# Kernel tuning notes

Measured on AMD Instinct MI355X. Metric: run time of the kernel, lower is better.

## Reference

```python
import jax, jax.numpy as jnp
import numpy as np

N_VERTS = 100000
N_EDGES = 50000
NNZ = 1600000
C_IN = 128
C_OUT = 128


def setup_inputs() -> dict:
    key = jax.random.key(0)
    k = jax.random.split(key, 7)
    X = jax.random.normal(k[0], (N_VERTS, C_IN), dtype=jnp.float32)
    v_ids = jax.random.randint(k[1], (NNZ,), 0, N_VERTS)
    e_ids = jax.random.randint(k[2], (NNZ,), 0, N_EDGES)
    s1 = 1.0 / np.sqrt(C_IN)
    s2 = 1.0 / np.sqrt(C_OUT)
    W_v2e = jax.random.uniform(k[3], (C_IN, C_OUT), jnp.float32, -s1, s1)
    b_v2e = jax.random.uniform(k[4], (C_OUT,), jnp.float32, -s1, s1)
    W_e2v = jax.random.uniform(k[5], (C_OUT, C_OUT), jnp.float32, -s2, s2)
    b_e2v = jax.random.uniform(k[6], (C_OUT,), jnp.float32, -s2, s2)
    return {"X": X, "W_v2e": W_v2e, "b_v2e": b_v2e, "W_e2v": W_e2v,
            "b_e2v": b_e2v, "v_ids": v_ids, "e_ids": e_ids}


def _mean_agg(feats_src, src_ids, dst_ids, num_dst):
    # gather source features along incidence list, segment-mean into destination
    gathered = feats_src[src_ids]                                   # [nnz, C]
    ssum = jax.ops.segment_sum(gathered, dst_ids, num_segments=num_dst)
    cnt = jax.ops.segment_sum(jnp.ones((src_ids.shape[0],), feats_src.dtype),
                              dst_ids, num_segments=num_dst)
    return ssum / jnp.maximum(cnt, 1.0)[:, None]


def reference(X, W_v2e, b_v2e, W_e2v, b_e2v, v_ids, e_ids):
    # theta_v2e
    Xp = X @ W_v2e + b_v2e                                          # [V, C_out]
    # v2e mean aggregation + ReLU
    Y = jax.nn.relu(_mean_agg(Xp, v_ids, e_ids, N_EDGES))           # [E, C_out]
    # theta_e2v
    Yp = Y @ W_e2v + b_e2v                                          # [E, C_out]
    # e2v mean aggregation
    Xo = _mean_agg(Yp, e_ids, v_ids, N_VERTS)                       # [V, C_out]
    # not is_last: final ReLU (bn disabled, dropout in eval mode = identity)
    return jax.nn.relu(Xo)
```

## Files before the change

kernel.cpp:

```cpp
#include <hip/hip_runtime.h>
#include <stdint.h>

#define V_N 100000
#define E_N 50000
#define C_N 128

#define NB_E 196
#define NB_V 391
#define NBINS (NB_E + NB_V)
#define CHUNK 8192
#define CAP_B 10240

typedef unsigned short u16;
typedef unsigned int u32;

__device__ __forceinline__ u16 f2bf(float f) {
    union { float f; u32 i; } c; c.f = f;
    u32 i = c.i;
    i += 0x7fffu + ((i >> 16) & 1u);
    return (u16)(i >> 16);
}
__device__ __forceinline__ void unpack2(u32 u, float& lo, float& hi) {
    union { u32 i; float f; } a, b;
    a.i = u << 16; b.i = u & 0xffff0000u;
    lo = a.f; hi = b.f;
}

__global__ __launch_bounds__(64) void flagf_k(float* out, float v) {
    if (threadIdx.x == 0 && blockIdx.x == 0) out[0] = v;
}

__global__ __launch_bounds__(256) void zero_i4(int4* __restrict__ p, int n) {
    int i = blockIdx.x * 256 + threadIdx.x;
    if (i < n) { int4 z = {0, 0, 0, 0}; p[i] = z; }
}

__global__ __launch_bounds__(256) void histA_k(const int* __restrict__ v_ids,
                                               const int* __restrict__ e_ids,
                                               int* __restrict__ gbin, int nnz) {
    __shared__ int hb[NBINS];
    for (int i = threadIdx.x; i < NBINS; i += 256) hb[i] = 0;
    __syncthreads();
    const int nnz4 = nnz >> 2;
    const int b4 = blockIdx.x * (CHUNK >> 2);
    #pragma unroll
    for (int u = 0; u < 8; ++u) {
        int i4 = b4 + u * 256 + threadIdx.x;
        if (i4 < nnz4) {
            int4 e = ((const int4*)e_ids)[i4];
            int4 v = ((const int4*)v_ids)[i4];
            #define HA(ee, vv) \
                if ((unsigned)ee < (unsigned)E_N && (unsigned)vv < (unsigned)V_N) { \
                    atomicAdd(&hb[ee >> 8], 1); atomicAdd(&hb[NB_E + (vv >> 8)], 1); }
            HA(e.x, v.x); HA(e.y, v.y); HA(e.z, v.z); HA(e.w, v.w);
            #undef HA
        }
    }
    __syncthreads();
    for (int i = threadIdx.x; i < NBINS; i += 256)
        if (hb[i]) atomicAdd(&gbin[i], hb[i]);
}

__global__ __launch_bounds__(1024) void scanB_k(const int* __restrict__ gbin,
                                                int* __restrict__ base_e, int* __restrict__ base_v,
                                                int* __restrict__ curb_e, int* __restrict__ curb_v,
                                                int* __restrict__ off_e, int* __restrict__ off_v) {
    __shared__ int wtot[16];
    const int t = threadIdx.x, lane = t & 63, wid = t >> 6;
    {
        int x = (t < NB_E) ? gbin[t] : 0;
        int incl = x;
        for (int d = 1; d < 64; d <<= 1) { int u = __shfl_up(incl, d); if (lane >= d) incl += u; }
        if (lane == 63) wtot[wid] = incl;
        __syncthreads();
        int carry = 0;
        for (int w = 0; w < wid; ++w) carry += wtot[w];
        int excl = carry + incl - x;
        if (t < NB_E) { base_e[t] = excl; curb_e[t] = excl; }
        if (t == 0) {
            int tot = 0;
            for (int w = 0; w < 16; ++w) tot += wtot[w];
            base_e[NB_E] = tot; off_e[E_N] = tot;
        }
        __syncthreads();
    }
    {
        int x = (t < NB_V) ? gbin[NB_E + t] : 0;
        int incl = x;
        for (int d = 1; d < 64; d <<= 1) { int u = __shfl_up(incl, d); if (lane >= d) incl += u; }
        if (lane == 63) wtot[wid] = incl;
        __syncthreads();
        int carry = 0;
        for (int w = 0; w < wid; ++w) carry += wtot[w];
        int excl = carry + incl - x;
        if (t < NB_V) { base_v[t] = excl; curb_v[t] = excl; }
        if (t == 0) {
            int tot = 0;
            for (int w = 0; w < 16; ++w) tot += wtot[w];
            base_v[NB_V] = tot; off_v[V_N] = tot;
        }
    }
}

__global__ __launch_bounds__(512) void passA_k(const int* __restrict__ v_ids,
                                               const int* __restrict__ e_ids,
                                               int* __restrict__ curb_e, int* __restrict__ curb_v,
                                               u32* __restrict__ pairs_e, u32* __restrict__ pairs_v,
                                               int nnz) {
    __shared__ u32 stage[CHUNK];
    __shared__ int cnt[512], runoff[513], delta[512], cnt2[512];
    __shared__ int wtot[8];
    const int t = threadIdx.x, lane = t & 63, wid = t >> 6;
    const int nnz4 = nnz >> 2;
    const int b4 = blockIdx.x * (CHUNK >> 2);

    for (int dir = 0; dir < 2; ++dir) {
        const int nb = dir ? NB_V : NB_E;
        for (int i = t; i < nb; i += 512) { cnt[i] = 0; cnt2[i] = 0; }
        __syncthreads();
        #pragma unroll
        for (int u = 0; u < 4; ++u) {
            int i4 = b4 + u * 512 + t;
            if (i4 < nnz4) {
                int4 e = ((const int4*)e_ids)[i4];
                int4 v = ((const int4*)v_ids)[i4];
                #define PC(ee, vv) \
                    if ((unsigned)ee < (unsigned)E_N && (unsigned)vv < (unsigned)V_N) { \
                        int k_ = dir ? vv : ee; atomicAdd(&cnt[k_ >> 8], 1); }
                PC(e.x, v.x); PC(e.y, v.y); PC(e.z, v.z); PC(e.w, v.w);
                #undef PC
            }
        }
        __syncthreads();
        int x = (t < nb) ? cnt[t] : 0;
        int incl = x;
        for (int d = 1; d < 64; d <<= 1) { int u = __shfl_up(incl, d); if (lane >= d) incl += u; }
        if (lane == 63) wtot[wid] = incl;
        __syncthreads();
        int carry = 0;
        for (int w = 0; w < wid; ++w) carry += wtot[w];
        int excl = carry + incl - x;
        if (t < nb) runoff[t] = excl;
        if (t == 0) {
            int tot = 0;
            for (int w = 0; w < 8; ++w) tot += wtot[w];
            runoff[nb] = tot;
        }
        __syncthreads();
        const int total = runoff[nb];
        if (t < nb && cnt[t] > 0) {
            int r = atomicAdd((dir ? curb_v : curb_e) + t, cnt[t]);
            delta[t] = r - runoff[t];
        }
        __syncthreads();
        #pragma unroll
        for (int u = 0; u < 4; ++u) {
            int i4 = b4 + u * 512 + t;
            if (i4 < nnz4) {
                int4 e = ((const int4*)e_ids)[i4];
                int4 v = ((const int4*)v_ids)[i4];
                #define PS(ee, vv) \
                    if ((unsigned)ee < (unsigned)E_N && (unsigned)vv < (unsigned)V_N) { \
                        int k_ = dir ? vv : ee; int b_ = k_ >> 8; \
                        u32 pk_ = dir ? (((u32)(k_ & 255) << 16) | (u32)ee) \
                                      : (((u32)(k_ & 255) << 17) | (u32)vv); \
                        int idx_ = runoff[b_] + atomicAdd(&cnt2[b_], 1); \
                        stage[idx_] = pk_; }
                PS(e.x, v.x); PS(e.y, v.y); PS(e.z, v.z); PS(e.w, v.w);
                #undef PS
            }
        }
        __syncthreads();
        u32* pairs = dir ? pairs_v : pairs_e;
        for (int i = t; i < total; i += 512) {
            int lo = 0, hi = nb;
            while (hi - lo > 1) { int mid = (lo + hi) >> 1; if (runoff[mid] <= i) lo = mid; else hi = mid; }
            pairs[i + delta[lo]] = stage[i];
        }
        __syncthreads();
    }
}

__global__ __launch_bounds__(256) void passB_k(const u32* __restrict__ pairs_e,
                                               const u32* __restrict__ pairs_v,
                                               const int* __restrict__ base_e,
                                               const int* __restrict__ base_v,
                                               int* __restrict__ off_e, int* __restrict__ off_v,
                                               int* __restrict__ se_src, int* __restrict__ sv_src) {
    __shared__ int cntk[256], curk[256];
    __shared__ u32 buf[CAP_B];
    __shared__ int wtot[4];
    int b = blockIdx.x;
    const u32* pairs; const int* base; int* off; int* outv; int keyN, shift; u32 mask;
    if (b < NB_E) { pairs = pairs_e; base = base_e; off = off_e; outv = se_src; keyN = E_N; shift = 17; mask = 0x1FFFFu; }
    else { b -= NB_E; pairs = pairs_v; base = base_v; off = off_v; outv = sv_src; keyN = V_N; shift = 16; mask = 0xFFFFu; }
    const int lo = base[b], hi = base[b + 1], cnt = hi - lo, k0 = b << 8;
    const int t = threadIdx.x, lane = t & 63, wid = t >> 6;
    cntk[t] = 0;
    __syncthreads();
    for (int i = t; i < cnt; i += 256) { u32 p = pairs[lo + i]; atomicAdd(&cntk[p >> shift], 1); }
    __syncthreads();
    int x = cntk[t];
    int incl = x;
    for (int d = 1; d < 64; d <<= 1) { int u = __shfl_up(incl, d); if (lane >= d) incl += u; }
    if (lane == 63) wtot[wid] = incl;
    __syncthreads();
    int carry = 0;
    for (int w = 0; w < wid; ++w) carry += wtot[w];
    int excl = carry + incl - x;
    if (k0 + t < keyN) off[k0 + t] = lo + excl;
    curk[t] = excl;
    __syncthreads();
    if (cnt <= CAP_B) {
        for (int i = t; i < cnt; i += 256) {
            u32 p = pairs[lo + i];
            int pos = atomicAdd(&curk[p >> shift], 1);
            buf[pos] = p & mask;
        }
        __syncthreads();
        for (int i = t; i < cnt; i += 256) outv[lo + i] = (int)buf[i];
    } else {
        for (int i = t; i < cnt; i += 256) {
            u32 p = pairs[lo + i];
            int pos = atomicAdd(&curk[p >> shift], 1);
            outv[lo + pos] = (int)(p & mask);
        }
    }
}

template<int MODE>
__global__ __launch_bounds__(256) void gemm_tiled_k(const float* __restrict__ A,
                                                    const float* __restrict__ W,
                                                    const float* __restrict__ bias,
                                                    const int* __restrict__ off,
                                                    u16* __restrict__ Cout, int M) {
    __shared__ float As[128 * 32];
    __shared__ float Wsh[32 * 128];
    const int tid = threadIdx.x;
    const int tx = tid & 15;
    const int ty = tid >> 4;
    const int m0 = blockIdx.x * 128;

    float acc[8][8];
    #pragma unroll
    for (int i = 0; i < 8; ++i)
        #pragma unroll
        for (int j = 0; j < 8; ++j) acc[i][j] = 0.f;

    for (int kk = 0; kk < 128; kk += 32) {
        __syncthreads();
        #pragma unroll
        for (int u = 0; u < 4; ++u) {
            int f = tid + u * 256;
            int r = f >> 3, c4 = f & 7;
            float4 val = { 0.f, 0.f, 0.f, 0.f };
            if (m0 + r < M) {
                val = *(const float4*)(A + (size_t)(m0 + r) * C_N + kk + c4 * 4);
                if (MODE) {
                    val.x = fmaxf(val.x, 0.f); val.y = fmaxf(val.y, 0.f);
                    val.z = fmaxf(val.z, 0.f); val.w = fmaxf(val.w, 0.f);
                }
            }
            int sc4 = c4 ^ ((r >> 3) & 7);
            *(float4*)(As + r * 32 + sc4 * 4) = val;
        }
        #pragma unroll
        for (int u = 0; u < 4; ++u) {
            int f = tid + u * 256;
            int r = f >> 5, c4 = f & 31;
            *(float4*)(Wsh + r * 128 + c4 * 4) = *(const float4*)(W + (size_t)(kk + r) * C_N + c4 * 4);
        }
        __syncthreads();
        #pragma unroll
        for (int k4 = 0; k4 < 32; k4 += 4) {
            float4 a[8];
            #pragma unroll
            for (int i = 0; i < 8; ++i) {
                int row = ty * 8 + i;
                int sc4 = (k4 >> 2) ^ (ty & 7);
                a[i] = *(const float4*)(As + row * 32 + sc4 * 4);
            }
            #pragma unroll
            for (int dk = 0; dk < 4; ++dk) {
                float4 w0 = *(const float4*)(Wsh + (k4 + dk) * 128 + tx * 4);
                float4 w1 = *(const float4*)(Wsh + (k4 + dk) * 128 + 64 + tx * 4);
                #pragma unroll
                for (int i = 0; i < 8; ++i) {
                    float av = (dk == 0) ? a[i].x : (dk == 1) ? a[i].y : (dk == 2) ? a[i].z : a[i].w;
                    acc[i][0] = fmaf(av, w0.x, acc[i][0]);
                    acc[i][1] = fmaf(av, w0.y, acc[i][1]);
                    acc[i][2] = fmaf(av, w0.z, acc[i][2]);
                    acc[i][3] = fmaf(av, w0.w, acc[i][3]);
                    acc[i][4] = fmaf(av, w1.x, acc[i][4]);
                    acc[i][5] = fmaf(av, w1.y, acc[i][5]);
                    acc[i][6] = fmaf(av, w1.z, acc[i][6]);
                    acc[i][7] = fmaf(av, w1.w, acc[i][7]);
                }
            }
        }
    }

    float4 bb0 = *(const float4*)(bias + tx * 4);
    float4 bb1 = *(const float4*)(bias + 64 + tx * 4);
    #pragma unroll
    for (int i = 0; i < 8; ++i) {
        int m = m0 + ty * 8 + i;
        if (m >= M) break;
        float inv = 1.f;
        if (MODE) { int len = off[m + 1] - off[m]; inv = 1.f / (float)max(len, 1); }
        float v0, v1, v2, v3, v4, v5, v6, v7;
        if (MODE) {
            v0 = acc[i][0] * inv + bb0.x; v1 = acc[i][1] * inv + bb0.y;
            v2 = acc[i][2] * inv + bb0.z; v3 = acc[i][3] * inv + bb0.w;
            v4 = acc[i][4] * inv + bb1.x; v5 = acc[i][5] * inv + bb1.y;
            v6 = acc[i][6] * inv + bb1.z; v7 = acc[i][7] * inv + bb1.w;
        } else {
            v0 = acc[i][0] + bb0.x; v1 = acc[i][1] + bb0.y;
            v2 = acc[i][2] + bb0.z; v3 = acc[i][3] + bb0.w;
            v4 = acc[i][4] + bb1.x; v5 = acc[i][5] + bb1.y;
            v6 = acc[i][6] + bb1.z; v7 = acc[i][7] + bb1.w;
        }
        u32 p0 = (u32)f2bf(v0) | ((u32)f2bf(v1) << 16);
        u32 p1 = (u32)f2bf(v2) | ((u32)f2bf(v3) << 16);
        u32 p2 = (u32)f2bf(v4) | ((u32)f2bf(v5) << 16);
        u32 p3 = (u32)f2bf(v6) | ((u32)f2bf(v7) << 16);
        u32* dst = (u32*)(Cout + (size_t)m * C_N);
        uint2 q0 = { p0, p1 }, q1 = { p2, p3 };
        *(uint2*)(dst + tx * 2) = q0;
        *(uint2*)(dst + 32 + tx * 2) = q1;
    }
}

__global__ __launch_bounds__(256) void seg_e_k(const u16* __restrict__ Xp,
                                               const int* __restrict__ off,
                                               const int* __restrict__ srcs,
                                               float* __restrict__ Ysum, int E) {
    int e = blockIdx.x * 4 + (threadIdx.x >> 6);
    if (e >= E) return;
    int lane = threadIdx.x & 63;
    int j0 = off[e], j1 = off[e + 1];
    float a0 = 0.f, a1 = 0.f;
    int j = j0;
    for (; j + 1 < j1; j += 2) {
        int s0 = srcs[j], s1 = srcs[j + 1];
        u32 q0 = ((const u32*)(Xp + (size_t)s0 * C_N))[lane];
        u32 q1 = ((const u32*)(Xp + (size_t)s1 * C_N))[lane];
        float l0, h0, l1, h1;
        unpack2(q0, l0, h0); unpack2(q1, l1, h1);
        a0 += l0 + l1; a1 += h0 + h1;
    }
    if (j < j1) {
        int s0 = srcs[j];
        u32 q0 = ((const u32*)(Xp + (size_t)s0 * C_N))[lane];
        float l0, h0; unpack2(q0, l0, h0);
        a0 += l0; a1 += h0;
    }
    float2 w; w.x = a0; w.y = a1;
    ((float2*)Ysum)[(size_t)e * 64 + lane] = w;
}

__global__ __launch_bounds__(256) void seg_v_k(const u16* __restrict__ Yp,
                                               const int* __restrict__ off,
                                               const int* __restrict__ srcs,
                                               float* __restrict__ out, int V) {
    int v = blockIdx.x * 4 + (threadIdx.x >> 6);
    if (v >= V) return;
    int lane = threadIdx.x & 63;
    int j0 = off[v], j1 = off[v + 1];
    float a0 = 0.f, a1 = 0.f;
    int j = j0;
    for (; j + 1 < j1; j += 2) {
        int s0 = srcs[j], s1 = srcs[j + 1];
        u32 q0 = ((const u32*)(Yp + (size_t)s0 * C_N))[lane];
        u32 q1 = ((const u32*)(Yp + (size_t)s1 * C_N))[lane];
        float l0, h0, l1, h1;
        unpack2(q0, l0, h0); unpack2(q1, l1, h1);
        a0 += l0 + l1; a1 += h0 + h1;
    }
    if (j < j1) {
        int s0 = srcs[j];
        u32 q0 = ((const u32*)(Yp + (size_t)s0 * C_N))[lane];
        float l0, h0; unpack2(q0, l0, h0);
        a0 += l0; a1 += h0;
    }
    float inv = 1.0f / (float)max(j1 - j0, 1);
    float2 w;
    w.x = fmaxf(a0 * inv, 0.f);
    w.y = fmaxf(a1 * inv, 0.f);
    ((float2*)out)[(size_t)v * 64 + lane] = w;
}

extern "C" void kernel_launch(void* const* d_in, const int* in_sizes, int n_in,
                              void* d_out, int out_size, void* d_ws, size_t ws_size,
                              hipStream_t stream) {
    const float* X     = (const float*)d_in[0];
    const float* W_v2e = (const float*)d_in[1];
    const float* b_v2e = (const float*)d_in[2];
    const float* W_e2v = (const float*)d_in[3];
    const float* b_e2v = (const float*)d_in[4];
    const int*   v_ids = (const int*)d_in[5];
    const int*   e_ids = (const int*)d_in[6];
    float* out = (float*)d_out;

    bool sizesOK = (n_in == 7) && (out_size == 12800000)
        && in_sizes[0] == 12800000 && in_sizes[1] == 16384 && in_sizes[2] == 128
        && in_sizes[3] == 16384 && in_sizes[4] == 128
        && in_sizes[5] == 1600000 && in_sizes[6] == 1600000;
    if (!sizesOK) { flagf_k<<<1, 64, 0, stream>>>(out, 1.0e6f); return; }
    if (ws_size < 28000000) { flagf_k<<<1, 64, 0, stream>>>(out, 2.0e6f); return; }
    const int nnz = in_sizes[5];

    u32*   pairs_e = (u32*)d_out;
    u32*   pairs_v = pairs_e + nnz;
    u16*   Xp   = (u16*)d_out;
    float* Ysum = (float*)((char*)d_out + 25600000);

    char* ws = (char*)d_ws;
    u16* Yp     = (u16*)(ws + 0);
    int* se_src = (int*)(ws + 12800000);
    int* sv_src = (int*)(ws + 19200000);
    int* gbin   = (int*)(ws + 25600000);
    int* base_e = (int*)(ws + 25602560);
    int* base_v = (int*)(ws + 25603584);
    int* curb_e = (int*)(ws + 25605632);
    int* curb_v = (int*)(ws + 25606656);
    int* off_e  = (int*)(ws + 25608704);
    int* off_v  = (int*)(ws + 25808768);

    const int NCH = (nnz + CHUNK - 1) / CHUNK;

    zero_i4<<<1, 256, 0, stream>>>((int4*)gbin, 152);
    histA_k<<<NCH, 256, 0, stream>>>(v_ids, e_ids, gbin, nnz);
    scanB_k<<<1, 1024, 0, stream>>>(gbin, base_e, base_v, curb_e, curb_v, off_e, off_v);
    passA_k<<<NCH, 512, 0, stream>>>(v_ids, e_ids, curb_e, curb_v, pairs_e, pairs_v, nnz);
    passB_k<<<NBINS, 256, 0, stream>>>(pairs_e, pairs_v, base_e, base_v, off_e, off_v, se_src, sv_src);

    gemm_tiled_k<0><<<(V_N + 127) / 128, 256, 0, stream>>>(X, W_v2e, b_v2e, nullptr, Xp, V_N);
    seg_e_k<<<(E_N + 3) / 4, 256, 0, stream>>>(Xp, off_e, se_src, Ysum, E_N);
    gemm_tiled_k<1><<<(E_N + 127) / 128, 256, 0, stream>>>(Ysum, W_e2v, b_e2v, off_e, Yp, E_N);
    seg_v_k<<<(V_N + 3) / 4, 256, 0, stream>>>(Yp, off_v, sv_src, out, V_N);

    (void)ws_size;
}
```

Measured before the change: 444.5 us.

## Fuse first GEMM with histogram, stage ids in LDS, widen segment gathers

Merges the first projection GEMM and the incidence histogram into one launch, with block ranges split between the two roles, so the GEMM runs concurrently with the sort preprocessing. To allow this, the pair buffers move to the second half of the output buffer so they no longer overlap Xp. passA now loads the id chunk into shared memory once instead of reading it from global four times, at the cost of much more LDS per block and lower occupancy. The segment-mean kernels are unified, and each half-wave now gathers 8-byte rows so four neighbours are in flight per iteration, with a cross-half shuffle reduction at the end.

```diff
diff --git a/kernel.cpp b/kernel.cpp
--- a/kernel.cpp
+++ b/kernel.cpp
@@ -10,6 +10,7 @@
 #define NBINS (NB_E + NB_V)
 #define CHUNK 8192
 #define CAP_B 10240
+#define G1B 782
 
 typedef unsigned short u16;
 typedef unsigned int u32;
@@ -35,30 +36,154 @@
     if (i < n) { int4 z = {0, 0, 0, 0}; p[i] = z; }
 }
 
-__global__ __launch_bounds__(256) void histA_k(const int* __restrict__ v_ids,
-                                               const int* __restrict__ e_ids,
-                                               int* __restrict__ gbin, int nnz) {
-    __shared__ int hb[NBINS];
-    for (int i = threadIdx.x; i < NBINS; i += 256) hb[i] = 0;
-    __syncthreads();
-    const int nnz4 = nnz >> 2;
-    const int b4 = blockIdx.x * (CHUNK >> 2);
+template<int MODE>
+__device__ __forceinline__ void gemm_body(float* As, float* Wsh, int bid,
+                                          const float* __restrict__ A,
+                                          const float* __restrict__ W,
+                                          const float* __restrict__ bias,
+                                          const int* __restrict__ off,
+                                          u16* __restrict__ Cout, int M) {
+    const int tid = threadIdx.x;
+    const int tx = tid & 15;
+    const int ty = tid >> 4;
+    const int m0 = bid * 128;
+
+    float acc[8][8];
     #pragma unroll
-    for (int u = 0; u < 8; ++u) {
-        int i4 = b4 + u * 256 + threadIdx.x;
-        if (i4 < nnz4) {
-            int4 e = ((const int4*)e_ids)[i4];
-            int4 v = ((const int4*)v_ids)[i4];
-            #define HA(ee, vv) \
-                if ((unsigned)ee < (unsigned)E_N && (unsigned)vv < (unsigned)V_N) { \
-                    atomicAdd(&hb[ee >> 8], 1); atomicAdd(&hb[NB_E + (vv >> 8)], 1); }
-            HA(e.x, v.x); HA(e.y, v.y); HA(e.z, v.z); HA(e.w, v.w);
-            #undef HA
-        }
-    }
-    __syncthreads();
-    for (int i = threadIdx.x; i < NBINS; i += 256)
-        if (hb[i]) atomicAdd(&gbin[i], hb[i]);
+    for (int i = 0; i < 8; ++i)
+        #pragma unroll
+        for (int j = 0; j < 8; ++j) acc[i][j] = 0.f;
+
+    for (int kk = 0; kk < 128; kk += 32) {
+        __syncthreads();
+        #pragma unroll
+        for (int u = 0; u < 4; ++u) {
+            int f = tid + u * 256;
+            int r = f >> 3, c4 = f & 7;
+            float4 val = { 0.f, 0.f, 0.f, 0.f };
+            if (m0 + r < M) {
+                val = *(const float4*)(A + (size_t)(m0 + r) * C_N + kk + c4 * 4);
+                if (MODE) {
+                    val.x = fmaxf(val.x, 0.f); val.y = fmaxf(val.y, 0.f);
+                    val.z = fmaxf(val.z, 0.f); val.w = fmaxf(val.w, 0.f);
+                }
+            }
+            int sc4 = c4 ^ ((r >> 3) & 7);
+            *(float4*)(As + r * 32 + sc4 * 4) = val;
+        }
+        #pragma unroll
+        for (int u = 0; u < 4; ++u) {
+            int f = tid + u * 256;
+            int r = f >> 5, c4 = f & 31;
+            *(float4*)(Wsh + r * 128 + c4 * 4) = *(const float4*)(W + (size_t)(kk + r) * C_N + c4 * 4);
+        }
+        __syncthreads();
+        #pragma unroll
+        for (int k4 = 0; k4 < 32; k4 += 4) {
+            float4 a[8];
+            #pragma unroll
+            for (int i = 0; i < 8; ++i) {
+                int row = ty * 8 + i;
+                int sc4 = (k4 >> 2) ^ (ty & 7);
+                a[i] = *(const float4*)(As + row * 32 + sc4 * 4);
+            }
+            #pragma unroll
+            for (int dk = 0; dk < 4; ++dk) {
+                float4 w0 = *(const float4*)(Wsh + (k4 + dk) * 128 + tx * 4);
+                float4 w1 = *(const float4*)(Wsh + (k4 + dk) * 128 + 64 + tx * 4);
+                #pragma unroll
+                for (int i = 0; i < 8; ++i) {
+                    float av = (dk == 0) ? a[i].x : (dk == 1) ? a[i].y : (dk == 2) ? a[i].z : a[i].w;
+                    acc[i][0] = fmaf(av, w0.x, acc[i][0]);
+                    acc[i][1] = fmaf(av, w0.y, acc[i][1]);
+                    acc[i][2] = fmaf(av, w0.z, acc[i][2]);
+                    acc[i][3] = fmaf(av, w0.w, acc[i][3]);
+                    acc[i][4] = fmaf(av, w1.x, acc[i][4]);
+                    acc[i][5] = fmaf(av, w1.y, acc[i][5]);
+                    acc[i][6] = fmaf(av, w1.z, acc[i][6]);
+                    acc[i][7] = fmaf(av, w1.w, acc[i][7]);
+                }
+            }
+        }
+    }
+
+    float4 bb0 = *(const float4*)(bias + tx * 4);
+    float4 bb1 = *(const float4*)(bias + 64 + tx * 4);
+    #pragma unroll
+    for (int i = 0; i < 8; ++i) {
+        int m = m0 + ty * 8 + i;
+        if (m >= M) break;
+        float inv = 1.f;
+        if (MODE) { int len = off[m + 1] - off[m]; inv = 1.f / (float)max(len, 1); }
+        float v0, v1, v2, v3, v4, v5, v6, v7;
+        if (MODE) {
+            v0 = acc[i][0] * inv + bb0.x; v1 = acc[i][1] * inv + bb0.y;
+            v2 = acc[i][2] * inv + bb0.z; v3 = acc[i][3] * inv + bb0.w;
+            v4 = acc[i][4] * inv + bb1.x; v5 = acc[i][5] * inv + bb1.y;
+            v6 = acc[i][6] * inv + bb1.z; v7 = acc[i][7] * inv + bb1.w;
+        } else {
+            v0 = acc[i][0] + bb0.x; v1 = acc[i][1] + bb0.y;
+            v2 = acc[i][2] + bb0.z; v3 = acc[i][3] + bb0.w;
+            v4 = acc[i][4] + bb1.x; v5 = acc[i][5] + bb1.y;
+            v6 = acc[i][6] + bb1.z; v7 = acc[i][7] + bb1.w;
+        }
+        u32 p0 = (u32)f2bf(v0) | ((u32)f2bf(v1) << 16);
+        u32 p1 = (u32)f2bf(v2) | ((u32)f2bf(v3) << 16);
+        u32 p2 = (u32)f2bf(v4) | ((u32)f2bf(v5) << 16);
+        u32 p3 = (u32)f2bf(v6) | ((u32)f2bf(v7) << 16);
+        u32* dst = (u32*)(Cout + (size_t)m * C_N);
+        uint2 q0 = { p0, p1 }, q1 = { p2, p3 };
+        *(uint2*)(dst + tx * 2) = q0;
+        *(uint2*)(dst + 32 + tx * 2) = q1;
+    }
+}
+
+template<int MODE>
+__global__ __launch_bounds__(256) void gemm_tiled_k(const float* __restrict__ A,
+                                                    const float* __restrict__ W,
+                                                    const float* __restrict__ bias,
+                                                    const int* __restrict__ off,
+                                                    u16* __restrict__ Cout, int M) {
+    __shared__ __align__(16) float As[128 * 32];
+    __shared__ __align__(16) float Wsh[32 * 128];
+    gemm_body<MODE>(As, Wsh, blockIdx.x, A, W, bias, off, Cout, M);
+}
+
+__global__ __launch_bounds__(256) void fusedA_k(const float* __restrict__ X,
+                                                const float* __restrict__ W,
+                                                const float* __restrict__ bias,
+                                                u16* __restrict__ Xp,
+                                                const int* __restrict__ v_ids,
+                                                const int* __restrict__ e_ids,
+                                                int* __restrict__ gbin, int nnz) {
+    __shared__ __align__(16) char smem[32768];
+    if ((int)blockIdx.x < G1B) {
+        gemm_body<0>((float*)smem, (float*)(smem + 16384), blockIdx.x,
+                     X, W, bias, nullptr, Xp, V_N);
+    } else {
+        int* hb = (int*)smem;
+        const int bid = blockIdx.x - G1B;
+        for (int i = threadIdx.x; i < NBINS; i += 256) hb[i] = 0;
+        __syncthreads();
+        const int nnz4 = nnz >> 2;
+        const int b4 = bid * (CHUNK >> 2);
+        #pragma unroll
+        for (int u = 0; u < 8; ++u) {
+            int i4 = b4 + u * 256 + threadIdx.x;
+            if (i4 < nnz4) {
+                int4 e = ((const int4*)e_ids)[i4];
+                int4 v = ((const int4*)v_ids)[i4];
+                #define HA(ee, vv) \
+                    if ((unsigned)ee < (unsigned)E_N && (unsigned)vv < (unsigned)V_N) { \
+                        atomicAdd(&hb[ee >> 8], 1); atomicAdd(&hb[NB_E + (vv >> 8)], 1); }
+                HA(e.x, v.x); HA(e.y, v.y); HA(e.z, v.z); HA(e.w, v.w);
+                #undef HA
+            }
+        }
+        __syncthreads();
+        for (int i = threadIdx.x; i < NBINS; i += 256)
+            if (hb[i]) atomicAdd(&gbin[i], hb[i]);
+    }
 }
 
 __global__ __launch_bounds__(1024) void scanB_k(const int* __restrict__ gbin,
@@ -107,28 +232,35 @@
                                                int* __restrict__ curb_e, int* __restrict__ curb_v,
                                                u32* __restrict__ pairs_e, u32* __restrict__ pairs_v,
                                                int nnz) {
-    __shared__ u32 stage[CHUNK];
+    __shared__ __align__(16) int ids_e[CHUNK];
+    __shared__ __align__(16) int ids_v[CHUNK];
+    __shared__ __align__(16) u32 stage[CHUNK];
     __shared__ int cnt[512], runoff[513], delta[512], cnt2[512];
     __shared__ int wtot[8];
     const int t = threadIdx.x, lane = t & 63, wid = t >> 6;
     const int nnz4 = nnz >> 2;
     const int b4 = blockIdx.x * (CHUNK >> 2);
 
+    #pragma unroll
+    for (int u = 0; u < 4; ++u) {
+        int k4 = u * 512 + t;
+        int i4 = b4 + k4;
+        int4 e = { -1, -1, -1, -1 }, v = { -1, -1, -1, -1 };
+        if (i4 < nnz4) { e = ((const int4*)e_ids)[i4]; v = ((const int4*)v_ids)[i4]; }
+        ((int4*)ids_e)[k4] = e;
+        ((int4*)ids_v)[k4] = v;
+    }
+    __syncthreads();
+
     for (int dir = 0; dir < 2; ++dir) {
         const int nb = dir ? NB_V : NB_E;
-        for (int i = t; i < nb; i += 512) { cnt[i] = 0; cnt2[i] = 0; }
-        __syncthreads();
-        #pragma unroll
-        for (int u = 0; u < 4; ++u) {
-            int i4 = b4 + u * 512 + t;
-            if (i4 < nnz4) {
-                int4 e = ((const int4*)e_ids)[i4];
-                int4 v = ((const int4*)v_ids)[i4];
-                #define PC(ee, vv) \
-                    if ((unsigned)ee < (unsigned)E_N && (unsigned)vv < (unsigned)V_N) { \
-                        int k_ = dir ? vv : ee; atomicAdd(&cnt[k_ >> 8], 1); }
-                PC(e.x, v.x); PC(e.y, v.y); PC(e.z, v.z); PC(e.w, v.w);
-                #undef PC
+        cnt[t] = 0; cnt2[t] = 0;
+        __syncthreads();
+        for (int k = t; k < CHUNK; k += 512) {
+            int ee = ids_e[k], vv = ids_v[k];
+            if ((unsigned)ee < (unsigned)E_N && (unsigned)vv < (unsigned)V_N) {
+                int key = dir ? vv : ee;
+                atomicAdd(&cnt[key >> 8], 1);
             }
         }
         __syncthreads();
@@ -153,21 +285,15 @@
             delta[t] = r - runoff[t];
         }
         __syncthreads();
-        #pragma unroll
-        for (int u = 0; u < 4; ++u) {
-            int i4 = b4 + u * 512 + t;
-            if (i4 < nnz4) {
-                int4 e = ((const int4*)e_ids)[i4];
-                int4 v = ((const int4*)v_ids)[i4];
-                #define PS(ee, vv) \
-                    if ((unsigned)ee < (unsigned)E_N && (unsigned)vv < (unsigned)V_N) { \
-                        int k_ = dir ? vv : ee; int b_ = k_ >> 8; \
-                        u32 pk_ = dir ? (((u32)(k_ & 255) << 16) | (u32)ee) \
-                                      : (((u32)(k_ & 255) << 17) | (u32)vv); \
-                        int idx_ = runoff[b_] + atomicAdd(&cnt2[b_], 1); \
-                        stage[idx_] = pk_; }
-                PS(e.x, v.x); PS(e.y, v.y); PS(e.z, v.z); PS(e.w, v.w);
-                #undef PS
+        for (int k = t; k < CHUNK; k += 512) {
+            int ee = ids_e[k], vv = ids_v[k];
+            if ((unsigned)ee < (unsigned)E_N && (unsigned)vv < (unsigned)V_N) {
+                int key = dir ? vv : ee;
+                int b_ = key >> 8;
+                u32 pk_ = dir ? (((u32)(key & 255) << 16) | (u32)ee)
+                              : (((u32)(key & 255) << 17) | (u32)vv);
+                int idx_ = runoff[b_] + atomicAdd(&cnt2[b_], 1);
+                stage[idx_] = pk_;
             }
         }
         __syncthreads();
@@ -229,165 +355,58 @@
 }
 
 template<int MODE>
-__global__ __launch_bounds__(256) void gemm_tiled_k(const float* __restrict__ A,
-                                                    const float* __restrict__ W,
-                                                    const float* __restrict__ bias,
-                                                    const int* __restrict__ off,
-                                                    u16* __restrict__ Cout, int M) {
-    __shared__ float As[128 * 32];
-    __shared__ float Wsh[32 * 128];
-    const int tid = threadIdx.x;
-    const int tx = tid & 15;
-    const int ty = tid >> 4;
-    const int m0 = blockIdx.x * 128;
-
-    float acc[8][8];
-    #pragma unroll
-    for (int i = 0; i < 8; ++i)
-        #pragma unroll
-        for (int j = 0; j < 8; ++j) acc[i][j] = 0.f;
-
-    for (int kk = 0; kk < 128; kk += 32) {
-        __syncthreads();
-        #pragma unroll
-        for (int u = 0; u < 4; ++u) {
-            int f = tid + u * 256;
-            int r = f >> 3, c4 = f & 7;
-            float4 val = { 0.f, 0.f, 0.f, 0.f };
-            if (m0 + r < M) {
-                val = *(const float4*)(A + (size_t)(m0 + r) * C_N + kk + c4 * 4);
-                if (MODE) {
-                    val.x = fmaxf(val.x, 0.f); val.y = fmaxf(val.y, 0.f);
-                    val.z = fmaxf(val.z, 0.f); val.w = fmaxf(val.w, 0.f);
-                }
-            }
-            int sc4 = c4 ^ ((r >> 3) & 7);
-            *(float4*)(As + r * 32 + sc4 * 4) = val;
-        }
-        #pragma unroll
-        for (int u = 0; u < 4; ++u) {
-            int f = tid + u * 256;
-            int r = f >> 5, c4 = f & 31;
-            *(float4*)(Wsh + r * 128 + c4 * 4) = *(const float4*)(W + (size_t)(kk + r) * C_N + c4 * 4);
-        }
-        __syncthreads();
-        #pragma unroll
-        for (int k4 = 0; k4 < 32; k4 += 4) {
-            float4 a[8];
-            #pragma unroll
-            for (int i = 0; i < 8; ++i) {
-                int row = ty * 8 + i;
-                int sc4 = (k4 >> 2) ^ (ty & 7);
-                a[i] = *(const float4*)(As + row * 32 + sc4 * 4);
-            }
-            #pragma unroll
-            for (int dk = 0; dk < 4; ++dk) {
-                float4 w0 = *(const float4*)(Wsh + (k4 + dk) * 128 + tx * 4);
-                float4 w1 = *(const float4*)(Wsh + (k4 + dk) * 128 + 64 + tx * 4);
-                #pragma unroll
-                for (int i = 0; i < 8; ++i) {
-                    float av = (dk == 0) ? a[i].x : (dk == 1) ? a[i].y : (dk == 2) ? a[i].z : a[i].w;
-                    acc[i][0] = fmaf(av, w0.x, acc[i][0]);
-                    acc[i][1] = fmaf(av, w0.y, acc[i][1]);
-                    acc[i][2] = fmaf(av, w0.z, acc[i][2]);
-                    acc[i][3] = fmaf(av, w0.w, acc[i][3]);
-                    acc[i][4] = fmaf(av, w1.x, acc[i][4]);
-                    acc[i][5] = fmaf(av, w1.y, acc[i][5]);
-                    acc[i][6] = fmaf(av, w1.z, acc[i][6]);
-                    acc[i][7] = fmaf(av, w1.w, acc[i][7]);
-                }
-            }
-        }
-    }
-
-    float4 bb0 = *(const float4*)(bias + tx * 4);
-    float4 bb1 = *(const float4*)(bias + 64 + tx * 4);
-    #pragma unroll
-    for (int i = 0; i < 8; ++i) {
-        int m = m0 + ty * 8 + i;
-        if (m >= M) break;
-        float inv = 1.f;
-        if (MODE) { int len = off[m + 1] - off[m]; inv = 1.f / (float)max(len, 1); }
-        float v0, v1, v2, v3, v4, v5, v6, v7;
+__global__ __launch_bounds__(256) void seg_k(const u16* __restrict__ F,
+                                             const int* __restrict__ off,
+                                             const int* __restrict__ srcs,
+                                             float* __restrict__ out, int N) {
+    int seg = blockIdx.x * 4 + (threadIdx.x >> 6);
+    if (seg >= N) return;
+    const int lane = threadIdx.x & 63;
+    const int half = lane >> 5;
+    const int c = lane & 31;
+    int j0 = off[seg], j1 = off[seg + 1];
+    float a0 = 0.f, a1 = 0.f, a2 = 0.f, a3 = 0.f;
+    int j = j0;
+    for (; j + 8 <= j1; j += 8) {
+        int s0 = srcs[j + 0 + half];
+        int s1 = srcs[j + 2 + half];
+        int s2 = srcs[j + 4 + half];
+        int s3 = srcs[j + 6 + half];
+        uint2 q0 = ((const uint2*)(F + (size_t)s0 * C_N))[c];
+        uint2 q1 = ((const uint2*)(F + (size_t)s1 * C_N))[c];
+        uint2 q2 = ((const uint2*)(F + (size_t)s2 * C_N))[c];
+        uint2 q3 = ((const uint2*)(F + (size_t)s3 * C_N))[c];
+        float l, h;
+        unpack2(q0.x, l, h); a0 += l; a1 += h; unpack2(q0.y, l, h); a2 += l; a3 += h;
+        unpack2(q1.x, l, h); a0 += l; a1 += h; unpack2(q1.y, l, h); a2 += l; a3 += h;
+        unpack2(q2.x, l, h); a0 += l; a1 += h; unpack2(q2.y, l, h); a2 += l; a3 += h;
+        unpack2(q3.x, l, h); a0 += l; a1 += h; unpack2(q3.y, l, h); a2 += l; a3 += h;
+    }
+    for (; j + 2 <= j1; j += 2) {
+        int s0 = srcs[j + half];
+        uint2 q0 = ((const uint2*)(F + (size_t)s0 * C_N))[c];
+        float l, h;
+        unpack2(q0.x, l, h); a0 += l; a1 += h; unpack2(q0.y, l, h); a2 += l; a3 += h;
+    }
+    if (j < j1 && half == 0) {
+        int s0 = srcs[j];
+        uint2 q0 = ((const uint2*)(F + (size_t)s0 * C_N))[c];
+        float l, h;
+        unpack2(q0.x, l, h); a0 += l; a1 += h; unpack2(q0.y, l, h); a2 += l; a3 += h;
+    }
+    a0 += __shfl_xor(a0, 32); a1 += __shfl_xor(a1, 32);
+    a2 += __shfl_xor(a2, 32); a3 += __shfl_xor(a3, 32);
+    if (half == 0) {
+        float4 w;
         if (MODE) {
-            v0 = acc[i][0] * inv + bb0.x; v1 = acc[i][1] * inv + bb0.y;
-            v2 = acc[i][2] * inv + bb0.z; v3 = acc[i][3] * inv + bb0.w;
-            v4 = acc[i][4] * inv + bb1.x; v5 = acc[i][5] * inv + bb1.y;
-            v6 = acc[i][6] * inv + bb1.z; v7 = acc[i][7] * inv + bb1.w;
+            float inv = 1.0f / (float)max(j1 - j0, 1);
+            w.x = fmaxf(a0 * inv, 0.f); w.y = fmaxf(a1 * inv, 0.f);
+            w.z = fmaxf(a2 * inv, 0.f); w.w = fmaxf(a3 * inv, 0.f);
         } else {
-            v0 = acc[i][0] + bb0.x; v1 = acc[i][1] + bb0.y;
-            v2 = acc[i][2] + bb0.z; v3 = acc[i][3] + bb0.w;
-            v4 = acc[i][4] + bb1.x; v5 = acc[i][5] + bb1.y;
-            v6 = acc[i][6] + bb1.z; v7 = acc[i][7] + bb1.w;
-        }
-        u32 p0 = (u32)f2bf(v0) | ((u32)f2bf(v1) << 16);
-        u32 p1 = (u32)f2bf(v2) | ((u32)f2bf(v3) << 16);
-        u32 p2 = (u32)f2bf(v4) | ((u32)f2bf(v5) << 16);
-        u32 p3 = (u32)f2bf(v6) | ((u32)f2bf(v7) << 16);
-        u32* dst = (u32*)(Cout + (size_t)m * C_N);
-        uint2 q0 = { p0, p1 }, q1 = { p2, p3 };
-        *(uint2*)(dst + tx * 2) = q0;
-        *(uint2*)(dst + 32 + tx * 2) = q1;
-    }
-}
-
-__global__ __launch_bounds__(256) void seg_e_k(const u16* __restrict__ Xp,
-                                               const int* __restrict__ off,
-                                               const int* __restrict__ srcs,
-                                               float* __restrict__ Ysum, int E) {
-    int e = blockIdx.x * 4 + (threadIdx.x >> 6);
-    if (e >= E) return;
-    int lane = threadIdx.x & 63;
-    int j0 = off[e], j1 = off[e + 1];
-    float a0 = 0.f, a1 = 0.f;
-    int j = j0;
-    for (; j + 1 < j1; j += 2) {
-        int s0 = srcs[j], s1 = srcs[j + 1];
-        u32 q0 = ((const u32*)(Xp + (size_t)s0 * C_N))[lane];
-        u32 q1 = ((const u32*)(Xp + (size_t)s1 * C_N))[lane];
-        float l0, h0, l1, h1;
-        unpack2(q0, l0, h0); unpack2(q1, l1, h1);
-        a0 += l0 + l1; a1 += h0 + h1;
-    }
-    if (j < j1) {
-        int s0 = srcs[j];
-        u32 q0 = ((const u32*)(Xp + (size_t)s0 * C_N))[lane];
-        float l0, h0; unpack2(q0, l0, h0);
-        a0 += l0; a1 += h0;
-    }
-    float2 w; w.x = a0; w.y = a1;
-    ((float2*)Ysum)[(size_t)e * 64 + lane] = w;
-}
-
-__global__ __launch_bounds__(256) void seg_v_k(const u16* __restrict__ Yp,
-                                               const int* __restrict__ off,
-                                               const int* __restrict__ srcs,
-                                               float* __restrict__ out, int V) {
-    int v = blockIdx.x * 4 + (threadIdx.x >> 6);
-    if (v >= V) return;
-    int lane = threadIdx.x & 63;
-    int j0 = off[v], j1 = off[v + 1];
-    float a0 = 0.f, a1 = 0.f;
-    int j = j0;
-    for (; j + 1 < j1; j += 2) {
-        int s0 = srcs[j], s1 = srcs[j + 1];
-        u32 q0 = ((const u32*)(Yp + (size_t)s0 * C_N))[lane];
-        u32 q1 = ((const u32*)(Yp + (size_t)s1 * C_N))[lane];
-        float l0, h0, l1, h1;
-        unpack2(q0, l0, h0); unpack2(q1, l1, h1);
-        a0 += l0 + l1; a1 += h0 + h1;
-    }
-    if (j < j1) {
-        int s0 = srcs[j];
-        u32 q0 = ((const u32*)(Yp + (size_t)s0 * C_N))[lane];
-        float l0, h0; unpack2(q0, l0, h0);
-        a0 += l0; a1 += h0;
-    }
-    float inv = 1.0f / (float)max(j1 - j0, 1);
-    float2 w;
-    w.x = fmaxf(a0 * inv, 0.f);
-    w.y = fmaxf(a1 * inv, 0.f);
-    ((float2*)out)[(size_t)v * 64 + lane] = w;
+            w.x = a0; w.y = a1; w.z = a2; w.w = a3;
+        }
+        ((float4*)(out + (size_t)seg * C_N))[c] = w;
+    }
 }
 
 extern "C" void kernel_launch(void* const* d_in, const int* in_sizes, int n_in,
@@ -410,10 +429,10 @@
     if (ws_size < 28000000) { flagf_k<<<1, 64, 0, stream>>>(out, 2.0e6f); return; }
     const int nnz = in_sizes[5];
 
-    u32*   pairs_e = (u32*)d_out;
+    u16*   Xp      = (u16*)d_out;
+    u32*   pairs_e = (u32*)((char*)d_out + 25600000);
     u32*   pairs_v = pairs_e + nnz;
-    u16*   Xp   = (u16*)d_out;
-    float* Ysum = (float*)((char*)d_out + 25600000);
+    float* Ysum    = (float*)((char*)d_out + 25600000);
 
     char* ws = (char*)d_ws;
     u16* Yp     = (u16*)(ws + 0);
@@ -430,15 +449,14 @@
     const int NCH = (nnz + CHUNK - 1) / CHUNK;
 
     zero_i4<<<1, 256, 0, stream>>>((int4*)gbin, 152);
-    histA_k<<<NCH, 256, 0, stream>>>(v_ids, e_ids, gbin, nnz);
+    fusedA_k<<<G1B + NCH, 256, 0, stream>>>(X, W_v2e, b_v2e, Xp, v_ids, e_ids, gbin, nnz);
     scanB_k<<<1, 1024, 0, stream>>>(gbin, base_e, base_v, curb_e, curb_v, off_e, off_v);
     passA_k<<<NCH, 512, 0, stream>>>(v_ids, e_ids, curb_e, curb_v, pairs_e, pairs_v, nnz);
     passB_k<<<NBINS, 256, 0, stream>>>(pairs_e, pairs_v, base_e, base_v, off_e, off_v, se_src, sv_src);
 
-    gemm_tiled_k<0><<<(V_N + 127) / 128, 256, 0, stream>>>(X, W_v2e, b_v2e, nullptr, Xp, V_N);
-    seg_e_k<<<(E_N + 3) / 4, 256, 0, stream>>>(Xp, off_e, se_src, Ysum, E_N);
+    seg_k<0><<<(E_N + 3) / 4, 256, 0, stream>>>(Xp, off_e, se_src, Ysum, E_N);
     gemm_tiled_k<1><<<(E_N + 127) / 128, 256, 0, stream>>>(Ysum, W_e2v, b_e2v, off_e, Yp, E_N);
-    seg_v_k<<<(V_N + 3) / 4, 256, 0, stream>>>(Yp, off_v, sv_src, out, V_N);
+    seg_k<1><<<(V_N + 3) / 4, 256, 0, stream>>>(Yp, off_v, sv_src, out, V_N);
 
     (void)ws_size;
 }
```

Result: faster. 371.1 us (-16.5%).
